# Optimization experiments

Measured on AMD Instinct MI355X. Metric: run time of the kernel, lower is better.

Reference implementation:

```python
import jax, jax.numpy as jnp
import numpy as np

HALF = 16  # num_outputs // 2 with num_features = 32
EPS = 1e-5


def _gmul(Wm, h):
    # Wm: [B,N,M,J], h: [B,M,F] -> [B,N,J*F] (j-major feature layout, matching torch split/cat/bmm)
    B, N = Wm.shape[0], Wm.shape[1]
    return jnp.einsum('bnmj,bmf->bnjf', Wm, h).reshape(B, N, -1)


def _bn(z, g, b):
    # training-mode BatchNorm2d on [R, C, 1, 1] == per-channel norm over rows, biased var
    m = z.mean(axis=0)
    v = z.var(axis=0)
    return g * (z - m) / jnp.sqrt(v + EPS) + b


def _block(W, hx, W_lg, hy, P, wx2x, wy2x, bx, wy2y, wx2y, by, gx, btx, gy, bty):
    B, N, M = P.shape[0], P.shape[1], P.shape[2]
    x2x = _gmul(W, hx).reshape(-1, wx2x.shape[0])
    y2x = _gmul(P, hy).reshape(-1, wy2x.shape[0])
    zx = x2x @ wx2x + y2x @ wy2x + bx
    zx = jnp.concatenate([jax.nn.relu(zx[:, :HALF]), zx[:, HALF:]], axis=1)
    xo = _bn(zx, gx, btx).reshape(B, N, -1)
    y2y = _gmul(W_lg, hy).reshape(-1, wy2y.shape[0])
    x2y = _gmul(jnp.swapaxes(P, 1, 2), hx).reshape(-1, wx2y.shape[0])
    zy = y2y @ wy2y + x2y @ wx2y + by
    zy = jnp.concatenate([jax.nn.relu(zy[:, :HALF]), zy[:, HALF:]], axis=1)
    yo = _bn(zy, gy, bty).reshape(B, M, -1)
    return xo, yo


def _forward(W, x, W_lg, y, P,
             wx2x0, wy2x0, bx0, wy2y0, wx2y0, by0, gx0, btx0, gy0, bty0,
             wx2x_m, wy2x_m, bx_m, wy2y_m, wx2y_m, by_m, gx_m, btx_m, gy_m, bty_m,
             wlx, wly, bl):
    hx, hy = _block(W, x, W_lg, y, P, wx2x0, wy2x0, bx0, wy2y0, wx2y0, by0,
                    gx0, btx0, gy0, bty0)
    for i in range(wx2x_m.shape[0]):  # fixed num_layers loop
        hx, hy = _block(W, hx, W_lg, hy, P,
                        wx2x_m[i], wy2x_m[i], bx_m[i], wy2y_m[i], wx2y_m[i], by_m[i],
                        gx_m[i], btx_m[i], gy_m[i], bty_m[i])
    # final layer: linear only, x branch output
    x2x = _gmul(W, hx).reshape(-1, wlx.shape[0])
    y2x = _gmul(P, hy).reshape(-1, wly.shape[0])
    out = (x2x @ wlx + y2x @ wly + bl).reshape(W.shape[0], W.shape[1], -1)
    return out


def setup_inputs() -> dict:
    key = jax.random.key(0)
    ks = iter(jax.random.split(key, 40))
    B, N, M, J, F, L, C = 1, 2048, 4096, 3, 32, 6, 2
    d = {}
    d['W'] = jax.random.normal(next(ks), (B, N, N, J), jnp.float32)
    d['x'] = jax.random.normal(next(ks), (B, N, 1), jnp.float32)
    d['W_lg'] = jax.random.normal(next(ks), (B, M, M, J), jnp.float32)
    d['y'] = jax.random.normal(next(ks), (B, M, 1), jnp.float32)
    d['P'] = jax.random.normal(next(ks), (B, N, M, 2), jnp.float32)
    s = 0.1
    d['wx2x0'] = jax.random.normal(next(ks), (J * 1, F), jnp.float32) * s
    d['wy2x0'] = jax.random.normal(next(ks), (2 * 1, F), jnp.float32) * s
    d['bx0'] = jax.random.normal(next(ks), (F,), jnp.float32) * s
    d['wy2y0'] = jax.random.normal(next(ks), (J * 1, F), jnp.float32) * s
    d['wx2y0'] = jax.random.normal(next(ks), (2 * 1, F), jnp.float32) * s
    d['by0'] = jax.random.normal(next(ks), (F,), jnp.float32) * s
    d['gx0'] = jnp.ones((F,), jnp.float32)
    d['btx0'] = jnp.zeros((F,), jnp.float32)
    d['gy0'] = jnp.ones((F,), jnp.float32)
    d['bty0'] = jnp.zeros((F,), jnp.float32)
    d['wx2x_m'] = jax.random.normal(next(ks), (L, J * F, F), jnp.float32) * s
    d['wy2x_m'] = jax.random.normal(next(ks), (L, 2 * F, F), jnp.float32) * s
    d['bx_m'] = jax.random.normal(next(ks), (L, F), jnp.float32) * s
    d['wy2y_m'] = jax.random.normal(next(ks), (L, J * F, F), jnp.float32) * s
    d['wx2y_m'] = jax.random.normal(next(ks), (L, 2 * F, F), jnp.float32) * s
    d['by_m'] = jax.random.normal(next(ks), (L, F), jnp.float32) * s
    d['gx_m'] = jnp.ones((L, F), jnp.float32)
    d['btx_m'] = jnp.zeros((L, F), jnp.float32)
    d['gy_m'] = jnp.ones((L, F), jnp.float32)
    d['bty_m'] = jnp.zeros((L, F), jnp.float32)
    d['wlx'] = jax.random.normal(next(ks), (J * F, C), jnp.float32) * s
    d['wly'] = jax.random.normal(next(ks), (2 * F, C), jnp.float32) * s
    d['bl'] = jax.random.normal(next(ks), (C,), jnp.float32) * s
    return d


def reference(W, x, W_lg, y, P,
              wx2x0, wy2x0, bx0, wy2y0, wx2y0, by0, gx0, btx0, gy0, bty0,
              wx2x_m, wy2x_m, bx_m, wy2y_m, wx2y_m, by_m, gx_m, btx_m, gy_m, bty_m,
              wlx, wly, bl):
    return _forward(W, x, W_lg, y, P,
                    wx2x0, wy2x0, bx0, wy2y0, wx2y0, by0, gx0, btx0, gy0, bty0,
                    wx2x_m, wy2x_m, bx_m, wy2y_m, wx2y_m, by_m, gx_m, btx_m, gy_m, bty_m,
                    wlx, wly, bl)
```

## Files before the change

kernel.cpp:

```cpp
#include <hip/hip_runtime.h>

typedef _Float16 f16x8 __attribute__((ext_vector_type(8)));
typedef float f32x4 __attribute__((ext_vector_type(4)));


__device__ inline unsigned short f16b(float v) {
    _Float16 h = (_Float16)v;
    return __builtin_bit_cast(unsigned short, h);
}

__device__ inline void atomAddF(float* p, float v) {
    __hip_atomic_fetch_add(p, v, __ATOMIC_RELAXED, __HIP_MEMORY_SCOPE_AGENT);
}

template<int K>
__device__ inline void pack_cvt(const float* __restrict__ src, unsigned short* __restrict__ dst, int u) {
    int o = u * 8;
    int panel = o / (K * 16);
    int rem = o - panel * (K * 16);
    int kstep = rem >> 9;
    int rem2 = rem & 511;
    int g = rem2 >> 7;
    int r15 = (rem2 >> 3) & 15;
    int row = (panel << 4) | r15;
    int k = (kstep << 5) | (g << 3);
    const float4* s = (const float4*)(src + (size_t)row * K + k);
    float4 v0 = s[0], v1 = s[1];
    uint4 q;
    q.x = (unsigned)f16b(v0.x) | ((unsigned)f16b(v0.y) << 16);
    q.y = (unsigned)f16b(v0.z) | ((unsigned)f16b(v0.w) << 16);
    q.z = (unsigned)f16b(v1.x) | ((unsigned)f16b(v1.y) << 16);
    q.w = (unsigned)f16b(v1.z) | ((unsigned)f16b(v1.w) << 16);
    ((uint4*)dst)[u] = q;
}

__global__ __launch_bounds__(256) void cvt_pack(const float* __restrict__ W, const float* __restrict__ P,
                                                const float* __restrict__ WL,
                                                unsigned short* __restrict__ Wb, unsigned short* __restrict__ Pb,
                                                unsigned short* __restrict__ WLb) {
    int u = blockIdx.x * 256 + threadIdx.x;
    if (u < 1572864) pack_cvt<6144>(W, Wb, u);
    else if (u < 1572864 + 2097152) pack_cvt<8192>(P, Pb, u - 1572864);
    else pack_cvt<12288>(WL, WLb, u - (1572864 + 2097152));
}

__global__ __launch_bounds__(256) void transpose_p(const float* __restrict__ P,
                                                   unsigned short* __restrict__ PT) {
    __shared__ unsigned int lds[64][33];
    int bid = blockIdx.x;
    int m0 = (bid & 127) * 32;
    int n0 = (bid >> 7) * 64;
    int tid = threadIdx.x;
    const float2* P2 = (const float2*)P;
    #pragma unroll
    for (int it = 0; it < 8; ++it) {
        int idx = it * 256 + tid;
        int nl = idx >> 5, ml = idx & 31;
        float2 v = P2[(size_t)(n0 + nl) * 4096 + (m0 + ml)];
        unsigned int pk = (unsigned int)f16b(v.x) | ((unsigned int)f16b(v.y) << 16);
        lds[nl][ml] = pk;
    }
    __syncthreads();
    unsigned int* PTu = (unsigned int*)PT;
    #pragma unroll
    for (int it = 0; it < 8; ++it) {
        int idx = it * 256 + tid;
        int ml = idx >> 6, nl = idx & 63;
        int row = m0 + ml;
        int k2 = (n0 + nl) * 2;
        int o = ((row >> 4) << 16) | ((k2 >> 5) << 9) | (((((k2 >> 3) & 3) << 4) | (row & 15)) << 3) | (k2 & 7);
        PTu[o >> 1] = lds[nl][ml];
    }
}

__global__ __launch_bounds__(256) void build_b(
    const float* __restrict__ srcx, const float* __restrict__ srcy,
    int Fin, int Fout, int buildB2, int use_bn,
    const float* __restrict__ stats,
    const float* __restrict__ gx, const float* __restrict__ btx,
    const float* __restrict__ gy, const float* __restrict__ bty,
    const float* __restrict__ w1a, const float* __restrict__ w1b,
    const float* __restrict__ w2a, const float* __restrict__ w2b,
    unsigned short* __restrict__ B1f, unsigned short* __restrict__ B2f) {
    int tid0 = blockIdx.x * 256 + threadIdx.x;
    const int NB1 = 14336 * 32;
    int isB2 = 0, t2 = tid0;
    if (tid0 >= NB1) {
        if (!buildB2) return;
        isB2 = 1; t2 = tid0 - NB1;
        if (t2 >= 16384 * 32) return;
    }
    int e = t2 & 7, lane = (t2 >> 3) & 63, hh = (t2 >> 9) & 1, t = t2 >> 10;
    int k = (t << 5) | ((lane >> 4) << 3) | e;
    int g = (hh << 4) | (lane & 15);
    float v = 0.f;
    if (g < Fout) {
        const float* hr; const float* wc; int useY;
        if (!isB2) {
            if (k < 6144) { int m = k / 3, j = k - 3 * m; hr = srcx + m * Fin; wc = w1a + (j * Fin) * Fout + g; useY = 0; }
            else { int k2 = k - 6144; int m = k2 >> 1, p = k2 & 1; hr = srcy + m * Fin; wc = w1b + (p * Fin) * Fout + g; useY = 1; }
        } else {
            if (k < 12288) { int m = k / 3, j = k - 3 * m; hr = srcy + m * Fin; wc = w2a + (j * Fin) * Fout + g; useY = 1; }
            else { int k2 = k - 12288; int n = k2 >> 1, p = k2 & 1; hr = srcx + n * Fin; wc = w2b + (p * Fin) * Fout + g; useY = 0; }
        }
        float a = 0.f;
        if (use_bn) {
            const float* st = useY ? stats + 64 : stats;
            const float* gv = useY ? gy : gx;
            const float* bv = useY ? bty : btx;
            float invn = useY ? (1.f / 4096.f) : (1.f / 2048.f);
            #pragma unroll
            for (int f = 0; f < 32; ++f) {
                float mean = st[f] * invn;
                float var = st[32 + f] * invn - mean * mean;
                float sc = gv[f] * rsqrtf(var + 1e-5f);
                float h = sc * (hr[f] - mean) + bv[f];
                a += h * wc[f * Fout];
            }
        } else {
            for (int f = 0; f < Fin; ++f) a += hr[f] * wc[f * Fout];
        }
        v = a;
    }
    if (!isB2) B1f[t2] = f16b(v); else B2f[t2] = f16b(v);
}

__global__ __launch_bounds__(256) void gemm_k(
    const unsigned short* __restrict__ Wb, const unsigned short* __restrict__ Pb,
    const unsigned short* __restrict__ WLb, const unsigned short* __restrict__ PTb,
    const unsigned short* __restrict__ B1f, const unsigned short* __restrict__ B2f,
    float* __restrict__ px, float* __restrict__ py, float* __restrict__ stats, int nwgx) {
    __shared__ float lds[4][1024];
    int bid = blockIdx.x;
    if (bid == 0 && threadIdx.x < 128) stats[threadIdx.x] = 0.f;
    const unsigned short* Bf;
    float* Z;
    int seg, Mbase, K, kloc, kb;
    const unsigned short* A16;
    if (bid < nwgx) {
        Bf = B1f;
        int mwg = bid / 14; seg = bid % 14;
        Mbase = mwg * 32;
        kb = seg << 10;
        Z = px + (size_t)seg * 65536;
        if (seg < 6) { K = 6144; kloc = kb;        A16 = Wb; }
        else         { K = 8192; kloc = kb - 6144; A16 = Pb; }
    } else {
        int b2 = bid - nwgx;
        Bf = B2f;
        int mwg = b2 / 16; seg = b2 % 16;
        Mbase = mwg * 32;
        kb = seg << 10;
        Z = py + (size_t)seg * 131072;
        if (seg < 12) { K = 12288; kloc = kb;         A16 = WLb; }
        else          { K = 4096;  kloc = kb - 12288; A16 = PTb; }
    }
    int wid = threadIdx.x >> 6, lane = threadIdx.x & 63;
    int kq = wid << 8;
    const unsigned short* ap0 = A16 + (size_t)(Mbase >> 4) * (K * 16)
                              + (size_t)((kloc + kq) >> 5) * 512 + lane * 8;
    const unsigned short* ap1 = ap0 + (size_t)K * 16;
    const unsigned short* bp = Bf + ((size_t)((kb + kq) >> 5)) * 1024 + lane * 8;
    f32x4 acc00 = {0.f,0.f,0.f,0.f}, acc01 = {0.f,0.f,0.f,0.f};
    f32x4 acc10 = {0.f,0.f,0.f,0.f}, acc11 = {0.f,0.f,0.f,0.f};
    #pragma unroll
    for (int ks = 0; ks < 8; ++ks) {
        f16x8 a0 = *(const f16x8*)ap0;
        f16x8 a1 = *(const f16x8*)ap1;
        f16x8 b0 = *(const f16x8*)bp;
        f16x8 b1 = *(const f16x8*)(bp + 512);
        acc00 = __builtin_amdgcn_mfma_f32_16x16x32_f16(a0, b0, acc00, 0, 0, 0);
        acc10 = __builtin_amdgcn_mfma_f32_16x16x32_f16(a1, b0, acc10, 0, 0, 0);
        acc01 = __builtin_amdgcn_mfma_f32_16x16x32_f16(a0, b1, acc01, 0, 0, 0);
        acc11 = __builtin_amdgcn_mfma_f32_16x16x32_f16(a1, b1, acc11, 0, 0, 0);
        ap0 += 512; ap1 += 512; bp += 1024;
    }
    int col = lane & 15, r0 = (lane >> 4) << 2;
    float* l = lds[wid];
    #pragma unroll
    for (int r = 0; r < 4; ++r) {
        l[(r0 + r) * 32 + col]            = acc00[r];
        l[(r0 + r) * 32 + col + 16]       = acc01[r];
        l[(r0 + r + 16) * 32 + col]       = acc10[r];
        l[(r0 + r + 16) * 32 + col + 16]  = acc11[r];
    }
    __syncthreads();
    int t = threadIdx.x;
    float4 a = ((const float4*)lds[0])[t];
    float4 b = ((const float4*)lds[1])[t];
    float4 c = ((const float4*)lds[2])[t];
    float4 d = ((const float4*)lds[3])[t];
    float4 s;
    s.x = (a.x + b.x) + (c.x + d.x);
    s.y = (a.y + b.y) + (c.y + d.y);
    s.z = (a.z + b.z) + (c.z + d.z);
    s.w = (a.w + b.w) + (c.w + d.w);
    ((float4*)(Z + (size_t)Mbase * 32))[t] = s;
}

__global__ __launch_bounds__(256) void reduce_stats(
    const float* __restrict__ px, const float* __restrict__ py,
    const float* __restrict__ bx, const float* __restrict__ by,
    float* __restrict__ zax, float* __restrict__ zay,
    float* __restrict__ stats) {
    __shared__ float lsum[4][8][8];
    int bid = blockIdx.x, tid = threadIdx.x;
    const float4* src; const float* bias; float4* dst; float* st; int nseg, i4, stride4;
    if (bid < 64) { src = (const float4*)px; bias = bx; dst = (float4*)zax; st = stats;      nseg = 14; i4 = bid * 256 + tid;        stride4 = 16384; }
    else          { src = (const float4*)py; bias = by; dst = (float4*)zay; st = stats + 64; nseg = 16; i4 = (bid - 64) * 256 + tid; stride4 = 32768; }
    float4 s = {0.f, 0.f, 0.f, 0.f};
    for (int g = 0; g < nseg; ++g) {
        float4 v = src[(size_t)g * stride4 + i4];
        s.x += v.x; s.y += v.y; s.z += v.z; s.w += v.w;
    }
    int c0 = (i4 & 7) * 4;
    float4 b4 = *(const float4*)(bias + c0);
    s.x += b4.x; s.y += b4.y; s.z += b4.z; s.w += b4.w;
    if (c0 < 16) {
        s.x = fmaxf(s.x, 0.f); s.y = fmaxf(s.y, 0.f);
        s.z = fmaxf(s.z, 0.f); s.w = fmaxf(s.w, 0.f);
    }
    dst[i4] = s;
    float4 s2 = {s.x * s.x, s.y * s.y, s.z * s.z, s.w * s.w};
    #pragma unroll
    for (int mask = 8; mask <= 32; mask <<= 1) {
        s.x += __shfl_xor(s.x, mask); s.y += __shfl_xor(s.y, mask);
        s.z += __shfl_xor(s.z, mask); s.w += __shfl_xor(s.w, mask);
        s2.x += __shfl_xor(s2.x, mask); s2.y += __shfl_xor(s2.y, mask);
        s2.z += __shfl_xor(s2.z, mask); s2.w += __shfl_xor(s2.w, mask);
    }
    int w = tid >> 6, ln = tid & 63;
    if (ln < 8) {
        lsum[w][ln][0] = s.x;  lsum[w][ln][1] = s.y;  lsum[w][ln][2] = s.z;  lsum[w][ln][3] = s.w;
        lsum[w][ln][4] = s2.x; lsum[w][ln][5] = s2.y; lsum[w][ln][6] = s2.z; lsum[w][ln][7] = s2.w;
    }
    __syncthreads();
    if (tid < 64) {
        int q = tid >> 3, e = tid & 7;
        float v = lsum[0][q][e] + lsum[1][q][e] + lsum[2][q][e] + lsum[3][q][e];
        int col = q * 4 + (e & 3);
        atomAddF((e < 4) ? &st[col] : &st[32 + col], v);
    }
}

__global__ __launch_bounds__(256) void out_final(const float* __restrict__ px,
                                                 const float* __restrict__ bl,
                                                 float* __restrict__ out) {
    int tid = blockIdx.x * 256 + threadIdx.x;
    if (tid < 4096) {
        int n = tid >> 1, c = tid & 1;
        float a = bl[c];
        for (int s = 0; s < 14; ++s) a += px[(size_t)s * 65536 + n * 32 + c];
        out[tid] = a;
    }
}

extern "C" void kernel_launch(void* const* d_in, const int* in_sizes, int n_in,
                              void* d_out, int out_size, void* d_ws, size_t ws_size,
                              hipStream_t stream) {
    const float* W    = (const float*)d_in[0];
    const float* x    = (const float*)d_in[1];
    const float* WL   = (const float*)d_in[2];
    const float* y    = (const float*)d_in[3];
    const float* P    = (const float*)d_in[4];
    const float* wx2x0 = (const float*)d_in[5];
    const float* wy2x0 = (const float*)d_in[6];
    const float* bx0   = (const float*)d_in[7];
    const float* wy2y0 = (const float*)d_in[8];
    const float* wx2y0 = (const float*)d_in[9];
    const float* by0   = (const float*)d_in[10];
    const float* gx0   = (const float*)d_in[11];
    const float* btx0  = (const float*)d_in[12];
    const float* gy0   = (const float*)d_in[13];
    const float* bty0  = (const float*)d_in[14];
    const float* wx2x_m = (const float*)d_in[15];
    const float* wy2x_m = (const float*)d_in[16];
    const float* bx_m   = (const float*)d_in[17];
    const float* wy2y_m = (const float*)d_in[18];
    const float* wx2y_m = (const float*)d_in[19];
    const float* by_m   = (const float*)d_in[20];
    const float* gx_m   = (const float*)d_in[21];
    const float* btx_m  = (const float*)d_in[22];
    const float* gy_m   = (const float*)d_in[23];
    const float* bty_m  = (const float*)d_in[24];
    const float* wlx = (const float*)d_in[25];
    const float* wly = (const float*)d_in[26];
    const float* bl  = (const float*)d_in[27];

    char* base = (char*)d_ws;
    unsigned short* Wb  = (unsigned short*)(base + 0);
    unsigned short* Pb  = (unsigned short*)(base + 25165824);
    unsigned short* WLb = (unsigned short*)(base + 58720256);
    unsigned short* PTb = (unsigned short*)(base + 159383552);
    unsigned short* B1f = (unsigned short*)(base + 192937984);
    unsigned short* B2f = (unsigned short*)(base + 193855488);
    float* zax   = (float*)(base + 194904064);
    float* zay   = (float*)(base + 195166208);
    float* stats = (float*)(base + 195690496);
    float* px    = (float*)(base + 195691008);
    float* py    = (float*)(base + 199361024);

    cvt_pack<<<38912, 256, 0, stream>>>(W, P, WL, Wb, Pb, WLb);
    transpose_p<<<4096, 256, 0, stream>>>(P, PTb);

    build_b<<<3840, 256, 0, stream>>>(x, y, 1, 32, 1, 0, nullptr, nullptr, nullptr, nullptr, nullptr,
                                      wx2x0, wy2x0, wy2y0, wx2y0, B1f, B2f);
    gemm_k<<<2944, 256, 0, stream>>>(Wb, Pb, WLb, PTb, B1f, B2f, px, py, stats, 896);
    reduce_stats<<<192, 256, 0, stream>>>(px, py, bx0, by0, zax, zay, stats);

    for (int i = 0; i < 6; ++i) {
        const float* gv  = (i == 0) ? gx0  : gx_m  + (i - 1) * 32;
        const float* bv  = (i == 0) ? btx0 : btx_m + (i - 1) * 32;
        const float* gvy = (i == 0) ? gy0  : gy_m  + (i - 1) * 32;
        const float* bvy = (i == 0) ? bty0 : bty_m + (i - 1) * 32;
        build_b<<<3840, 256, 0, stream>>>(zax, zay, 32, 32, 1, 1, stats, gv, bv, gvy, bvy,
                                          wx2x_m + i * 3072, wy2x_m + i * 2048,
                                          wy2y_m + i * 3072, wx2y_m + i * 2048, B1f, B2f);
        gemm_k<<<2944, 256, 0, stream>>>(Wb, Pb, WLb, PTb, B1f, B2f, px, py, stats, 896);
        reduce_stats<<<192, 256, 0, stream>>>(px, py, bx_m + i * 32, by_m + i * 32, zax, zay, stats);
    }

    build_b<<<1792, 256, 0, stream>>>(zax, zay, 32, 2, 0, 1, stats,
                                      gx_m + 5 * 32, btx_m + 5 * 32, gy_m + 5 * 32, bty_m + 5 * 32,
                                      wlx, wly, nullptr, nullptr, B1f, B2f);
    gemm_k<<<896, 256, 0, stream>>>(Wb, Pb, WLb, PTb, B1f, B2f, px, py, stats, 896);
    out_final<<<16, 256, 0, stream>>>(px, bl, (float*)d_out);
}
```

Before: 683.1 us.

## Fuse P fp16 packing into transpose and precompute BN scale/shift once

The transpose kernel now also writes the row-major packed fp16 copy of P. P is therefore read from global memory once instead of being read by both cvt_pack and transpose_p, and cvt_pack becomes a grid-stride loop over only W and W_lg. The last reduce_stats block, found with an atomic counter, computes the per-channel BatchNorm scale and shift into the stats buffer. build_b then applies a single fused multiply-add per feature instead of recomputing mean, variance and rsqrt in every thread. This adds a counter, an acquire/release fence pattern and a larger stats region, which shifts the px/py offsets.

```diff
diff --git a/kernel.cpp b/kernel.cpp
--- a/kernel.cpp
+++ b/kernel.cpp
@@ -34,17 +34,17 @@
     ((uint4*)dst)[u] = q;
 }
 
-__global__ __launch_bounds__(256) void cvt_pack(const float* __restrict__ W, const float* __restrict__ P,
-                                                const float* __restrict__ WL,
-                                                unsigned short* __restrict__ Wb, unsigned short* __restrict__ Pb,
-                                                unsigned short* __restrict__ WLb) {
-    int u = blockIdx.x * 256 + threadIdx.x;
-    if (u < 1572864) pack_cvt<6144>(W, Wb, u);
-    else if (u < 1572864 + 2097152) pack_cvt<8192>(P, Pb, u - 1572864);
-    else pack_cvt<12288>(WL, WLb, u - (1572864 + 2097152));
+__global__ __launch_bounds__(256) void cvt_pack(const float* __restrict__ W, const float* __restrict__ WL,
+                                                unsigned short* __restrict__ Wb, unsigned short* __restrict__ WLb) {
+    const int NW = 1572864, TOT = 1572864 + 6291456;
+    for (int u = blockIdx.x * 256 + threadIdx.x; u < TOT; u += 2048 * 256) {
+        if (u < NW) pack_cvt<6144>(W, Wb, u);
+        else pack_cvt<12288>(WL, WLb, u - NW);
+    }
 }
 
 __global__ __launch_bounds__(256) void transpose_p(const float* __restrict__ P,
+                                                   unsigned short* __restrict__ Pb,
                                                    unsigned short* __restrict__ PT) {
     __shared__ unsigned int lds[64][33];
     int bid = blockIdx.x;
@@ -71,14 +71,22 @@
         int o = ((row >> 4) << 16) | ((k2 >> 5) << 9) | (((((k2 >> 3) & 3) << 4) | (row & 15)) << 3) | (k2 & 7);
         PTu[o >> 1] = lds[nl][ml];
     }
+    unsigned int* Pbu = (unsigned int*)Pb;
+    #pragma unroll
+    for (int it = 0; it < 8; ++it) {
+        int idx = it * 256 + tid;
+        int nl = idx >> 5, ml = idx & 31;
+        int row = n0 + nl;
+        int k = (m0 + ml) * 2;
+        int o = (row >> 4) * 131072 + ((k >> 5) << 9) + (((((k >> 3) & 3) << 4) | (row & 15)) << 3) + (k & 7);
+        Pbu[o >> 1] = lds[nl][ml];
+    }
 }
 
 __global__ __launch_bounds__(256) void build_b(
     const float* __restrict__ srcx, const float* __restrict__ srcy,
     int Fin, int Fout, int buildB2, int use_bn,
     const float* __restrict__ stats,
-    const float* __restrict__ gx, const float* __restrict__ btx,
-    const float* __restrict__ gy, const float* __restrict__ bty,
     const float* __restrict__ w1a, const float* __restrict__ w1b,
     const float* __restrict__ w2a, const float* __restrict__ w2b,
     unsigned short* __restrict__ B1f, unsigned short* __restrict__ B2f) {
@@ -105,16 +113,11 @@
         }
         float a = 0.f;
         if (use_bn) {
-            const float* st = useY ? stats + 64 : stats;
-            const float* gv = useY ? gy : gx;
-            const float* bv = useY ? bty : btx;
-            float invn = useY ? (1.f / 4096.f) : (1.f / 2048.f);
+            const float* sc = useY ? stats + 196 : stats + 132;
+            const float* sh = useY ? stats + 228 : stats + 164;
             #pragma unroll
             for (int f = 0; f < 32; ++f) {
-                float mean = st[f] * invn;
-                float var = st[32 + f] * invn - mean * mean;
-                float sc = gv[f] * rsqrtf(var + 1e-5f);
-                float h = sc * (hr[f] - mean) + bv[f];
+                float h = sc[f] * hr[f] + sh[f];
                 a += h * wc[f * Fout];
             }
         } else {
@@ -132,7 +135,7 @@
     float* __restrict__ px, float* __restrict__ py, float* __restrict__ stats, int nwgx) {
     __shared__ float lds[4][1024];
     int bid = blockIdx.x;
-    if (bid == 0 && threadIdx.x < 128) stats[threadIdx.x] = 0.f;
+    if (bid == 0 && threadIdx.x < 132) stats[threadIdx.x] = 0.f;
     const unsigned short* Bf;
     float* Z;
     int seg, Mbase, K, kloc, kb;
@@ -201,9 +204,12 @@
 __global__ __launch_bounds__(256) void reduce_stats(
     const float* __restrict__ px, const float* __restrict__ py,
     const float* __restrict__ bx, const float* __restrict__ by,
+    const float* __restrict__ gx, const float* __restrict__ btx,
+    const float* __restrict__ gy, const float* __restrict__ bty,
     float* __restrict__ zax, float* __restrict__ zay,
     float* __restrict__ stats) {
     __shared__ float lsum[4][8][8];
+    __shared__ int lastFlag;
     int bid = blockIdx.x, tid = threadIdx.x;
     const float4* src; const float* bias; float4* dst; float* st; int nseg, i4, stride4;
     if (bid < 64) { src = (const float4*)px; bias = bx; dst = (float4*)zax; st = stats;      nseg = 14; i4 = bid * 256 + tid;        stride4 = 16384; }
@@ -240,6 +246,27 @@
         float v = lsum[0][q][e] + lsum[1][q][e] + lsum[2][q][e] + lsum[3][q][e];
         int col = q * 4 + (e & 3);
         atomAddF((e < 4) ? &st[col] : &st[32 + col], v);
+    }
+    __syncthreads();
+    if (tid == 0) {
+        __threadfence();
+        int old = __hip_atomic_fetch_add((int*)(stats + 128), 1, __ATOMIC_ACQ_REL, __HIP_MEMORY_SCOPE_AGENT);
+        lastFlag = (old == 191) ? 1 : 0;
+    }
+    __syncthreads();
+    if (lastFlag && tid < 64) {
+        int f = tid & 31, isY = tid >> 5;
+        float* sb = stats + (isY ? 64 : 0);
+        float n = isY ? 4096.f : 2048.f;
+        float sum = __hip_atomic_load(&sb[f], __ATOMIC_RELAXED, __HIP_MEMORY_SCOPE_AGENT);
+        float ssq = __hip_atomic_load(&sb[32 + f], __ATOMIC_RELAXED, __HIP_MEMORY_SCOPE_AGENT);
+        float mean = sum / n;
+        float var = ssq / n - mean * mean;
+        const float* gv = isY ? gy : gx;
+        const float* bv = isY ? bty : btx;
+        float sc = gv[f] * rsqrtf(var + 1e-5f);
+        stats[132 + isY * 64 + f] = sc;
+        stats[164 + isY * 64 + f] = bv[f] - mean * sc;
     }
 }
 
@@ -297,31 +324,28 @@
     float* zax   = (float*)(base + 194904064);
     float* zay   = (float*)(base + 195166208);
     float* stats = (float*)(base + 195690496);
-    float* px    = (float*)(base + 195691008);
-    float* py    = (float*)(base + 199361024);
-
-    cvt_pack<<<38912, 256, 0, stream>>>(W, P, WL, Wb, Pb, WLb);
-    transpose_p<<<4096, 256, 0, stream>>>(P, PTb);
-
-    build_b<<<3840, 256, 0, stream>>>(x, y, 1, 32, 1, 0, nullptr, nullptr, nullptr, nullptr, nullptr,
+    float* px    = (float*)(base + 195692544);
+    float* py    = (float*)(base + 199362560);
+
+    cvt_pack<<<2048, 256, 0, stream>>>(W, WL, Wb, WLb);
+    transpose_p<<<4096, 256, 0, stream>>>(P, Pb, PTb);
+
+    build_b<<<3840, 256, 0, stream>>>(x, y, 1, 32, 1, 0, stats,
                                       wx2x0, wy2x0, wy2y0, wx2y0, B1f, B2f);
     gemm_k<<<2944, 256, 0, stream>>>(Wb, Pb, WLb, PTb, B1f, B2f, px, py, stats, 896);
-    reduce_stats<<<192, 256, 0, stream>>>(px, py, bx0, by0, zax, zay, stats);
+    reduce_stats<<<192, 256, 0, stream>>>(px, py, bx0, by0, gx0, btx0, gy0, bty0, zax, zay, stats);
 
     for (int i = 0; i < 6; ++i) {
-        const float* gv  = (i == 0) ? gx0  : gx_m  + (i - 1) * 32;
-        const float* bv  = (i == 0) ? btx0 : btx_m + (i - 1) * 32;
-        const float* gvy = (i == 0) ? gy0  : gy_m  + (i - 1) * 32;
-        const float* bvy = (i == 0) ? bty0 : bty_m + (i - 1) * 32;
-        build_b<<<3840, 256, 0, stream>>>(zax, zay, 32, 32, 1, 1, stats, gv, bv, gvy, bvy,
+        build_b<<<3840, 256, 0, stream>>>(zax, zay, 32, 32, 1, 1, stats,
                                           wx2x_m + i * 3072, wy2x_m + i * 2048,
                                           wy2y_m + i * 3072, wx2y_m + i * 2048, B1f, B2f);
         gemm_k<<<2944, 256, 0, stream>>>(Wb, Pb, WLb, PTb, B1f, B2f, px, py, stats, 896);
-        reduce_stats<<<192, 256, 0, stream>>>(px, py, bx_m + i * 32, by_m + i * 32, zax, zay, stats);
+        reduce_stats<<<192, 256, 0, stream>>>(px, py, bx_m + i * 32, by_m + i * 32,
+                                              gx_m + i * 32, btx_m + i * 32,
+                                              gy_m + i * 32, bty_m + i * 32, zax, zay, stats);
     }
 
     build_b<<<1792, 256, 0, stream>>>(zax, zay, 32, 2, 0, 1, stats,
-                                      gx_m + 5 * 32, btx_m + 5 * 32, gy_m + 5 * 32, bty_m + 5 * 32,
                                       wlx, wly, nullptr, nullptr, B1f, B2f);
     gemm_k<<<896, 256, 0, stream>>>(Wb, Pb, WLb, PTb, B1f, B2f, px, py, stats, 896);
     out_final<<<16, 256, 0, stream>>>(px, bl, (float*)d_out);
```

Measured after the change: 679.7 us. No clear change (-0.5%).
